# Kernel tuning notes

Measured on AMD Instinct MI355X. Metric: run time of the kernel, lower is better.

The kernel has to match this reference:

```python
import jax, jax.numpy as jnp
import numpy as np

B, N, D, H, DK = 4, 2048, 1024, 16, 64  # batch, seq, model_dim, heads, key_dim (= value_dim)
NEG = -1e9


def setup_inputs() -> dict:
    key = jax.random.key(0)
    ks = jax.random.split(key, 5)
    X = jax.random.normal(ks[0], (B, N, D), dtype=jnp.float32)
    # causal additive mask [N, N]; module slices mask[:N, :M] and adds to logits
    mask = jnp.where(jnp.tril(jnp.ones((N, N), dtype=bool)), 0.0, NEG).astype(jnp.float32)
    s = 1.0 / np.sqrt(D)
    Wq = jax.random.normal(ks[1], (D, H * DK), dtype=jnp.float32) * s
    Wk = jax.random.normal(ks[2], (D, H * DK), dtype=jnp.float32) * s
    Wv = jax.random.normal(ks[3], (D, H * DK), dtype=jnp.float32) * s
    Wo = jax.random.normal(ks[4], (H * DK, D), dtype=jnp.float32) * s
    return {"X": X, "mask": mask, "Wq": Wq, "Wk": Wk, "Wv": Wv, "Wo": Wo}


def reference(X, mask, Wq, Wk, Wv, Wo):
    # Linear projections (bias=False), then split heads: [B,N,H,DK] -> [B,H,N,DK]
    Q = (X @ Wq).reshape(B, N, H, DK).transpose(0, 2, 1, 3)
    K = (X @ Wk).reshape(B, N, H, DK).transpose(0, 2, 1, 3)
    V = (X @ Wv).reshape(B, N, H, DK).transpose(0, 2, 1, 3)
    # full [B,H,N,N] attention logits (module materializes it explicitly)
    att = jnp.einsum('bhnd,bhmd->bhnm', Q, K) / jnp.sqrt(jnp.float32(DK))
    # dropout is in eval mode here -> identity; then additive mask[:N,:M]
    att = att + mask[:N, :N]
    prob = jax.nn.softmax(att, axis=-1)
    values = jnp.einsum('bhnm,bhmd->bhnd', prob, V)
    values_cat = values.transpose(0, 2, 1, 3).reshape(B, N, H * DK)
    return values_cat @ Wo
```

## Files before the change

### kernel.cpp

```cpp
#include <hip/hip_runtime.h>

typedef __fp16   f2  __attribute__((ext_vector_type(2)));
typedef _Float16 h4  __attribute__((ext_vector_type(4)));
typedef _Float16 v8h __attribute__((ext_vector_type(8)));
typedef float    v4f __attribute__((ext_vector_type(4)));
struct f2x2 { f2 lo, hi; };

#if __has_builtin(__builtin_amdgcn_exp2f)
#define FEXP2(x) __builtin_amdgcn_exp2f(x)
#else
#define FEXP2(x) exp2f(x)
#endif

constexpr int Bn = 4, Nn = 2048, Dn = 1024, Hn = 16, DKn = 64, Mn = 8192;

__device__ __forceinline__ void load_lds16(const _Float16* g, _Float16* l) {
    __builtin_amdgcn_global_load_lds(
        (const __attribute__((address_space(1))) void*)g,
        (__attribute__((address_space(3))) void*)l, 16, 0, 0);
}

__global__ __launch_bounds__(256) void castAll(const float* __restrict__ x,
                                               _Float16* __restrict__ y,
                                               const float* __restrict__ Wq,
                                               const float* __restrict__ Wk,
                                               const float* __restrict__ Wv,
                                               const float* __restrict__ Wo,
                                               _Float16* __restrict__ Wqkv,
                                               _Float16* __restrict__ Wto) {
    __shared__ float tile[32][33];
    const int t = threadIdx.x;
    if (blockIdx.x < 8192) {
        const int i = blockIdx.x * 256 + t;
        const float4 v = ((const float4*)x)[i];
        h4 o; o[0] = (_Float16)v.x; o[1] = (_Float16)v.y;
        o[2] = (_Float16)v.z; o[3] = (_Float16)v.w;
        ((h4*)y)[i] = o;
        return;
    }
    const int wb = blockIdx.x - 8192;
    const int which = wb >> 10, bid = wb & 1023;
    const float* W = which == 0 ? Wq : which == 1 ? Wk : which == 2 ? Wv : Wo;
    _Float16* Dst = which < 3 ? (Wqkv + ((size_t)which << 20)) : Wto;
    const int bx = bid & 31, by = bid >> 5;
    const int r = t >> 3, c4 = (t & 7) * 4;
    const float4 v = *(const float4*)&W[(size_t)(by * 32 + r) * Dn + bx * 32 + c4];
    tile[r][c4 + 0] = v.x; tile[r][c4 + 1] = v.y;
    tile[r][c4 + 2] = v.z; tile[r][c4 + 3] = v.w;
    __syncthreads();
    h4 o;
    o[0] = (_Float16)tile[c4 + 0][r];
    o[1] = (_Float16)tile[c4 + 1][r];
    o[2] = (_Float16)tile[c4 + 2][r];
    o[3] = (_Float16)tile[c4 + 3][r];
    *(h4*)&Dst[(size_t)(bx * 32 + r) * Dn + by * 32 + c4] = o;
}

#define MFMA16(A, B, C) __builtin_amdgcn_mfma_f32_16x16x32_f16((A), (B), (C), 0, 0, 0)

__global__ __launch_bounds__(512, 2) void gemmqkv(const _Float16* __restrict__ A,
                                                  const _Float16* __restrict__ Wt,
                                                  _Float16* __restrict__ Qo,
                                                  _Float16* __restrict__ Ko,
                                                  _Float16* __restrict__ Vo)
{
    __shared__ __align__(16) _Float16 As[4 * 8192];
    __shared__ __align__(16) _Float16 Bs[4 * 6144];
    const int wgid = (blockIdx.x & 7) * 64 + (blockIdx.x >> 3);
    const int bx = wgid & 15, by = wgid >> 4;
    const int m0 = by * 256, n0 = bx * 192;
    const _Float16* Abase = A + (size_t)m0 * Dn;
    const _Float16* Bbase = Wt + (size_t)n0 * Dn;

    const int t = threadIdx.x, lane = t & 63, w = t >> 6;
    const int quad = lane >> 4, l16 = lane & 15;
    const int wm = w >> 2, wn = w & 3;
    const int rA = t >> 2;
    const int gc = ((t & 3) ^ ((t >> 3) & 3)) * 8;
    const _Float16* pA0 = Abase + (size_t)rA * Dn + gc;
    const _Float16* pA1 = pA0 + (size_t)128 * Dn;
    const _Float16* pB0 = Bbase + (size_t)rA * Dn + gc;
    const _Float16* pB1 = pB0 + (size_t)128 * Dn;
    auto stageA = [&](int ts, int sh) {
        const int reg = (ts & 1) * 2 + sh, ko = ts * 64 + sh * 32;
        load_lds16(pA0 + ko, As + reg * 8192 + w * 512);
        load_lds16(pA1 + ko, As + reg * 8192 + 4096 + w * 512);
    };
    auto stageB = [&](int ts, int sh) {
        const int reg = (ts & 1) * 2 + sh, ko = ts * 64 + sh * 32;
        load_lds16(pB0 + ko, Bs + reg * 6144 + w * 512);
        if (t < 256)
            load_lds16(pB1 + ko, Bs + reg * 6144 + 4096 + w * 512);
    };
    const int swz  = (quad ^ ((l16 >> 1) & 3)) * 8;
    const int aoff = (wm * 128 + l16) * 32 + swz;
    const int boff = (wn * 48 + l16) * 32 + swz;

    v4f acc[8][3];
#pragma unroll
    for (int i = 0; i < 8; ++i)
#pragma unroll
        for (int j = 0; j < 3; ++j) acc[i][j] = v4f{0.f, 0.f, 0.f, 0.f};

    stageA(0, 0); stageB(0, 0); stageA(0, 1); stageB(0, 1); stageA(1, 0); stageB(1, 0);
    asm volatile("s_waitcnt vmcnt(6)" ::: "memory");
    __builtin_amdgcn_s_barrier();

#define QKV_KSTEP(REG, TS, SH, DOST, VM, DOVM) do {                              \
    const _Float16* Ab_ = As + (REG) * 8192 + aoff;                              \
    const _Float16* Bb_ = Bs + (REG) * 6144 + boff;                              \
    v8h aL[4], aH[4], bL[3];                                                     \
    _Pragma("unroll") for (int q2 = 0; q2 < 4; ++q2)                             \
        aL[q2] = *(const v8h*)(Ab_ + q2 * 512);                                  \
    _Pragma("unroll") for (int q2 = 0; q2 < 3; ++q2)                             \
        bL[q2] = *(const v8h*)(Bb_ + q2 * 512);                                  \
    if (DOST) stageA((TS), (SH));                                                \
    __builtin_amdgcn_s_barrier();                                                \
    asm volatile("s_waitcnt lgkmcnt(0)" ::: "memory");                           \
    __builtin_amdgcn_s_setprio(1);                                               \
    _Pragma("unroll") for (int i2 = 0; i2 < 4; ++i2)                             \
        _Pragma("unroll") for (int j2 = 0; j2 < 3; ++j2)                         \
            acc[i2][j2] = MFMA16(aL[i2], bL[j2], acc[i2][j2]);                   \
    __builtin_amdgcn_s_setprio(0);                                               \
    __builtin_amdgcn_s_barrier();                                                \
    _Pragma("unroll") for (int q2 = 0; q2 < 4; ++q2)                             \
        aH[q2] = *(const v8h*)(Ab_ + 2048 + q2 * 512);                           \
    if (DOST) stageB((TS), (SH));                                                \
    __builtin_amdgcn_s_barrier();                                                \
    asm volatile("s_waitcnt lgkmcnt(0)" ::: "memory");                           \
    __builtin_amdgcn_s_setprio(1);                                               \
    _Pragma("unroll") for (int i2 = 0; i2 < 4; ++i2)                             \
        _Pragma("unroll") for (int j2 = 0; j2 < 3; ++j2)                         \
            acc[4 + i2][j2] = MFMA16(aH[i2], bL[j2], acc[4 + i2][j2]);           \
    __builtin_amdgcn_s_setprio(0);                                               \
    if (DOVM) asm volatile("s_waitcnt " VM ::: "memory");                        \
    __builtin_amdgcn_s_barrier();                                                \
} while (0)

    for (int tt = 0; tt < 14; tt += 2) {
        QKV_KSTEP(0, tt + 1, 1, true, "vmcnt(6)", true);
        QKV_KSTEP(1, tt + 2, 0, true, "vmcnt(6)", true);
        QKV_KSTEP(2, tt + 2, 1, true, "vmcnt(6)", true);
        QKV_KSTEP(3, tt + 3, 0, true, "vmcnt(6)", true);
    }
    QKV_KSTEP(0, 15, 1, true,  "vmcnt(6)", true);
    QKV_KSTEP(1, 0, 0, false, "vmcnt(3)", true);
    QKV_KSTEP(2, 0, 0, false, "vmcnt(0)", true);
    QKV_KSTEP(3, 0, 0, false, "vmcnt(0)", false);
#undef QKV_KSTEP

#pragma unroll
    for (int mf = 0; mf < 8; ++mf) {
        const int mbase = m0 + wm * 128 + mf * 16 + quad * 4;
        const int b = mbase >> 11, nr = mbase & (Nn - 1);
#pragma unroll
        for (int nf = 0; nf < 3; ++nf) {
            const int nG = n0 + wn * 48 + nf * 16 + l16;
            const int sec = nG >> 10, nl = nG & 1023;
            const int h = nl >> 6, dk = nl & 63;
            if (sec < 2) {
                _Float16* C = sec ? Ko : Qo;
                const float scale = sec ? 1.0f : 0.125f * 1.44269504f;
#pragma unroll
                for (int r = 0; r < 4; ++r)
                    C[((size_t)(b * Hn + h) * Nn + (nr + r)) * DKn + dk] =
                        (_Float16)(acc[mf][nf][r] * scale);
            } else {
                h4 o; o[0] = (_Float16)acc[mf][nf][0]; o[1] = (_Float16)acc[mf][nf][1];
                o[2] = (_Float16)acc[mf][nf][2]; o[3] = (_Float16)acc[mf][nf][3];
                *(h4*)&Vo[((size_t)(b * Hn + h) * DKn + dk) * Nn + nr] = o;
            }
        }
    }
}

__global__ __launch_bounds__(512, 2) void gemmo(const _Float16* __restrict__ A,
                                                const _Float16* __restrict__ Wt,
                                                float* __restrict__ C)
{
    __shared__ __align__(16) _Float16 As[4 * 8192];
    __shared__ __align__(16) _Float16 Bs[4 * 4096];
    const int wgid = (blockIdx.x & 7) * 32 + (blockIdx.x >> 3);
    const int bx = wgid & 7, by = wgid >> 3;
    const int m0 = by * 256, n0 = bx * 128;
    const _Float16* Abase = A + (size_t)m0 * Dn;
    const _Float16* Bbase = Wt + (size_t)n0 * Dn;

    const int t = threadIdx.x, lane = t & 63, w = t >> 6;
    const int quad = lane >> 4, l16 = lane & 15;
    const int wm = w & 3, wn = w >> 2;
    const int rA = t >> 2;
    const int gc = ((t & 3) ^ ((t >> 3) & 3)) * 8;
    const _Float16* pA0 = Abase + (size_t)rA * Dn + gc;
    const _Float16* pA1 = pA0 + (size_t)128 * Dn;
    const _Float16* pB0 = Bbase + (size_t)rA * Dn + gc;
    auto stage3 = [&](int ts, int sh) {
        const int reg = (ts & 1) * 2 + sh, ko = ts * 64 + sh * 32;
        load_lds16(pA0 + ko, As + reg * 8192 + w * 512);
        load_lds16(pA1 + ko, As + reg * 8192 + 4096 + w * 512);
        load_lds16(pB0 + ko, Bs + reg * 4096 + w * 512);
    };
    const int swz  = (quad ^ ((l16 >> 1) & 3)) * 8;
    const int aoff = (wm * 64 + l16) * 32 + swz;
    const int boff = (wn * 64 + l16) * 32 + swz;

    v4f acc[4][4];
#pragma unroll
    for (int i = 0; i < 4; ++i)
#pragma unroll
        for (int j = 0; j < 4; ++j) acc[i][j] = v4f{0.f, 0.f, 0.f, 0.f};

    stage3(0, 0); stage3(0, 1); stage3(1, 0);
    asm volatile("s_waitcnt vmcnt(6)" ::: "memory");
    __builtin_amdgcn_s_barrier();

#define O_KSTEP(REG, TS, SH, DOST, VM, DOVM) do {                                \
    const _Float16* Ab_ = As + (REG) * 8192 + aoff;                              \
    const _Float16* Bb_ = Bs + (REG) * 4096 + boff;                              \
    v8h aL[4], bL[4];                                                            \
    _Pragma("unroll") for (int q2 = 0; q2 < 4; ++q2) {                           \
        aL[q2] = *(const v8h*)(Ab_ + q2 * 512);                                  \
        bL[q2] = *(const v8h*)(Bb_ + q2 * 512);                                  \
    }                                                                            \
    if (DOST) stage3((TS), (SH));                                                \
    __builtin_amdgcn_s_barrier();                                                \
    asm volatile("s_waitcnt lgkmcnt(0)" ::: "memory");                           \
    __builtin_amdgcn_s_setprio(1);                                               \
    _Pragma("unroll") for (int i2 = 0; i2 < 4; ++i2)                             \
        _Pragma("unroll") for (int j2 = 0; j2 < 4; ++j2)                         \
            acc[i2][j2] = MFMA16(aL[i2], bL[j2], acc[i2][j2]);                   \
    __builtin_amdgcn_s_setprio(0);                                               \
    if (DOVM) asm volatile("s_waitcnt " VM ::: "memory");                        \
    __builtin_amdgcn_s_barrier();                                                \
} while (0)

    for (int tt = 0; tt < 14; tt += 2) {
        O_KSTEP(0, tt + 1, 1, true, "vmcnt(6)", true);
        O_KSTEP(1, tt + 2, 0, true, "vmcnt(6)", true);
        O_KSTEP(2, tt + 2, 1, true, "vmcnt(6)", true);
        O_KSTEP(3, tt + 3, 0, true, "vmcnt(6)", true);
    }
    O_KSTEP(0, 15, 1, true,  "vmcnt(6)", true);
    O_KSTEP(1, 0, 0, false, "vmcnt(3)", true);
    O_KSTEP(2, 0, 0, false, "vmcnt(0)", true);
    O_KSTEP(3, 0, 0, false, "vmcnt(0)", false);
#undef O_KSTEP

#pragma unroll
    for (int mf = 0; mf < 4; ++mf) {
        const int mbase = m0 + wm * 64 + mf * 16 + quad * 4;
#pragma unroll
        for (int nf = 0; nf < 4; ++nf) {
            const int n = n0 + wn * 64 + nf * 16 + l16;
#pragma unroll
            for (int r = 0; r < 4; ++r)
                C[(size_t)(mbase + r) * Dn + n] = acc[mf][nf][r];
        }
    }
}

__global__ __launch_bounds__(256) void flashv5(const _Float16* __restrict__ Q,
                                               const _Float16* __restrict__ K,
                                               const _Float16* __restrict__ Vt,
                                               _Float16* __restrict__ O)
{
    __shared__ __align__(16) _Float16 KS[64 * 64];
    __shared__ __align__(16) _Float16 VS[64 * 64];
    __shared__ __align__(16) _Float16 Ps[4][32 * 64];

    const int t = threadIdx.x;
    const int lane = t & 63, w = t >> 6;
    const int quad = lane >> 4, l16 = lane & 15;
    const int bh = blockIdx.x & 63;
    const int pr = blockIdx.x >> 6;
    const int b = bh >> 4, h = bh & 15;

    const _Float16* Qg = Q  + (size_t)bh * Nn * DKn;
    const _Float16* Kg = K  + (size_t)bh * Nn * DKn;
    const _Float16* Vg = Vt + (size_t)bh * DKn * Nn;

    auto stage = [&](int kt) {
        const int k0 = kt * 64;
#pragma unroll
        for (int jj = 0; jj < 2; ++jj) {
            const int ci = jj * 256 + w * 64 + lane;
            const int r = ci >> 3, c = ci & 7;
            const int gc = (c ^ (r & 7)) * 8;
            load_lds16(Kg + (size_t)(k0 + r) * DKn + gc, &KS[(jj * 256 + w * 64) * 8]);
            load_lds16(Vg + (size_t)r * Nn + k0 + gc,    &VS[(jj * 256 + w * 64) * 8]);
        }
    };
#define SWZ(arr, r, c) (*(const v8h*)&(arr)[(r) * 64 + (((c) ^ ((r) & 7)) * 8)])

    v8h ones;
#pragma unroll
    for (int i = 0; i < 8; ++i) ones[i] = (_Float16)1.0f;

    _Float16* Op = O + (size_t)b * Nn * Dn + h * DKn;

    for (int pass = 0; pass < 2; ++pass) {
        const int qtile = pass ? pr : 15 - pr;
        const int qb = qtile * 128 + w * 32;

        v8h qf[2][2];
#pragma unroll
        for (int qq = 0; qq < 2; ++qq)
#pragma unroll
            for (int ks = 0; ks < 2; ++ks)
                qf[qq][ks] = *(const v8h*)&Qg[(size_t)(qb + qq * 16 + l16) * DKn + ks * 32 + quad * 8];

        v4f o[2][4];
#pragma unroll
        for (int mq = 0; mq < 2; ++mq)
#pragma unroll
            for (int nt = 0; nt < 4; ++nt) o[mq][nt] = v4f{0.f, 0.f, 0.f, 0.f};
        v4f ol[2] = {v4f{0.f, 0.f, 0.f, 0.f}, v4f{0.f, 0.f, 0.f, 0.f}};

        const int NKT  = 2 * qtile + 2;
        const int diag = 2 * qtile + (w >> 1);

        for (int kt = 0; kt < NKT; ++kt) {
            stage(kt);
            __syncthreads();
            if (kt <= diag) {
                const int k0 = kt * 64;
                auto ptile = [&](bool domask) {
#pragma unroll
                    for (int kk = 0; kk < 4; ++kk) {
                        v4f s0 = v4f{0.f, 0.f, 0.f, 0.f}, s1 = v4f{0.f, 0.f, 0.f, 0.f};
#pragma unroll
                        for (int ks = 0; ks < 2; ++ks) {
                            const v8h ak = SWZ(KS, kk * 16 + l16, ks * 4 + quad);
                            s0 = __builtin_amdgcn_mfma_f32_16x16x32_f16(ak, qf[0][ks], s0, 0, 0, 0);
                            s1 = __builtin_amdgcn_mfma_f32_16x16x32_f16(ak, qf[1][ks], s1, 0, 0, 0);
                        }
                        const int key0 = k0 + kk * 16 + quad * 4;
#pragma unroll
                        for (int qq = 0; qq < 2; ++qq) {
                            const v4f sv = qq ? s1 : s0;
                            const int q = qb + qq * 16 + l16;
                            float p[4];
#pragma unroll
                            for (int r = 0; r < 4; ++r) {
                                float x = sv[r];
                                if (domask) x = (key0 + r > q) ? -1e9f : x;
                                p[r] = FEXP2(x);
                            }
                            f2x2 pkr;
                            pkr.lo = __builtin_amdgcn_cvt_pkrtz(p[0], p[1]);
                            pkr.hi = __builtin_amdgcn_cvt_pkrtz(p[2], p[3]);
                            const h4 pk = __builtin_bit_cast(h4, pkr);
                            const int prow = qq * 16 + l16;
                            const int pch  = kk * 2 + (quad >> 1);
                            *(h4*)&Ps[w][prow * 64 + ((pch ^ (prow & 7)) * 8 + (quad & 1) * 4)] = pk;
                        }
                    }
#pragma unroll
                    for (int ks = 0; ks < 2; ++ks)
#pragma unroll
                        for (int mq = 0; mq < 2; ++mq) {
                            const int arow = mq * 16 + l16;
                            const int ach  = ks * 4 + quad;
                            const v8h a = *(const v8h*)&Ps[w][arow * 64 + ((ach ^ (arow & 7)) * 8)];
#pragma unroll
                            for (int nt = 0; nt < 4; ++nt) {
                                const v8h bvv = SWZ(VS, nt * 16 + l16, ks * 4 + quad);
                                o[mq][nt] = __builtin_amdgcn_mfma_f32_16x16x32_f16(a, bvv, o[mq][nt], 0, 0, 0);
                            }
                            ol[mq] = __builtin_amdgcn_mfma_f32_16x16x32_f16(a, ones, ol[mq], 0, 0, 0);
                        }
                };
                if (kt == diag) ptile(true); else ptile(false);
            }
            __syncthreads();
        }

#pragma unroll
        for (int mq = 0; mq < 2; ++mq)
#pragma unroll
            for (int r = 0; r < 4; ++r) {
                const float li = 1.0f / ol[mq][r];
                const int qrow = qb + mq * 16 + quad * 4 + r;
#pragma unroll
                for (int nt = 0; nt < 4; ++nt)
                    Op[(size_t)qrow * Dn + nt * 16 + l16] = (_Float16)(o[mq][nt][r] * li);
            }
    }
#undef SWZ
}

extern "C" void kernel_launch(void* const* d_in, const int* in_sizes, int n_in,
                              void* d_out, int out_size, void* d_ws, size_t ws_size,
                              hipStream_t stream)
{
    const float* X  = (const float*)d_in[0];
    const float* Wq = (const float*)d_in[2];
    const float* Wk = (const float*)d_in[3];
    const float* Wv = (const float*)d_in[4];
    const float* Wo = (const float*)d_in[5];

    char* ws = (char*)d_ws;
    _Float16* Xh   = (_Float16*)ws;
    _Float16* Wqkv = (_Float16*)(ws + (16u << 20));
    _Float16* Wto  = Wqkv + (3u << 20);
    _Float16* Qh   = Wto + (1u << 20);
    _Float16* Kh   = Qh + (size_t)Mn * Dn;
    _Float16* Vth  = Kh + (size_t)Mn * Dn;
    _Float16* Ah   = Vth + (size_t)Mn * Dn;

    castAll<<<12288, 256, 0, stream>>>(X, Xh, Wq, Wk, Wv, Wo, Wqkv, Wto);
    gemmqkv<<<512, 512, 0, stream>>>(Xh, Wqkv, Qh, Kh, Vth);
    flashv5<<<512, 256, 0, stream>>>(Qh, Kh, Vth, Ah);
    gemmo<<<256, 512, 0, stream>>>(Ah, Wto, (float*)d_out);
}
```

Measured before the change: 249.1 us.

## Double-buffer K/V tiles in flash attention with async LDS prefetch

Splits the K and V shared-memory tiles into two buffers and issues the global-to-LDS loads for the next key tile before computing on the current one. Partial vmcnt waits and raw barriers replace the full __syncthreads pair, so memory latency can overlap with the MFMA work. This doubles the K/V LDS footprint, which may lower occupancy. The hand-written waitcnt counts assume exactly four outstanding loads per stage.

```diff
diff --git a/kernel.cpp b/kernel.cpp
--- a/kernel.cpp
+++ b/kernel.cpp
@@ -264,8 +264,8 @@
                                                const _Float16* __restrict__ Vt,
                                                _Float16* __restrict__ O)
 {
-    __shared__ __align__(16) _Float16 KS[64 * 64];
-    __shared__ __align__(16) _Float16 VS[64 * 64];
+    __shared__ __align__(16) _Float16 KS[2][64 * 64];
+    __shared__ __align__(16) _Float16 VS[2][64 * 64];
     __shared__ __align__(16) _Float16 Ps[4][32 * 64];
 
     const int t = threadIdx.x;
@@ -279,15 +279,15 @@
     const _Float16* Kg = K  + (size_t)bh * Nn * DKn;
     const _Float16* Vg = Vt + (size_t)bh * DKn * Nn;
 
-    auto stage = [&](int kt) {
+    auto stage = [&](int kt, int buf) {
         const int k0 = kt * 64;
 #pragma unroll
         for (int jj = 0; jj < 2; ++jj) {
             const int ci = jj * 256 + w * 64 + lane;
             const int r = ci >> 3, c = ci & 7;
             const int gc = (c ^ (r & 7)) * 8;
-            load_lds16(Kg + (size_t)(k0 + r) * DKn + gc, &KS[(jj * 256 + w * 64) * 8]);
-            load_lds16(Vg + (size_t)r * Nn + k0 + gc,    &VS[(jj * 256 + w * 64) * 8]);
+            load_lds16(Kg + (size_t)(k0 + r) * DKn + gc, &KS[buf][(jj * 256 + w * 64) * 8]);
+            load_lds16(Vg + (size_t)r * Nn + k0 + gc,    &VS[buf][(jj * 256 + w * 64) * 8]);
         }
     };
 #define SWZ(arr, r, c) (*(const v8h*)&(arr)[(r) * 64 + (((c) ^ ((r) & 7)) * 8)])
@@ -319,18 +319,27 @@
         const int NKT  = 2 * qtile + 2;
         const int diag = 2 * qtile + (w >> 1);
 
+        stage(0, 0);
         for (int kt = 0; kt < NKT; ++kt) {
-            stage(kt);
-            __syncthreads();
+            const int cur = kt & 1;
+            if (kt + 1 < NKT) {
+                stage(kt + 1, cur ^ 1);
+                asm volatile("s_waitcnt vmcnt(4)" ::: "memory");
+            } else {
+                asm volatile("s_waitcnt vmcnt(0)" ::: "memory");
+            }
+            __builtin_amdgcn_s_barrier();
             if (kt <= diag) {
                 const int k0 = kt * 64;
+                const _Float16* KSc = KS[cur];
+                const _Float16* VSc = VS[cur];
                 auto ptile = [&](bool domask) {
 #pragma unroll
                     for (int kk = 0; kk < 4; ++kk) {
                         v4f s0 = v4f{0.f, 0.f, 0.f, 0.f}, s1 = v4f{0.f, 0.f, 0.f, 0.f};
 #pragma unroll
                         for (int ks = 0; ks < 2; ++ks) {
-                            const v8h ak = SWZ(KS, kk * 16 + l16, ks * 4 + quad);
+                            const v8h ak = SWZ(KSc, kk * 16 + l16, ks * 4 + quad);
                             s0 = __builtin_amdgcn_mfma_f32_16x16x32_f16(ak, qf[0][ks], s0, 0, 0, 0);
                             s1 = __builtin_amdgcn_mfma_f32_16x16x32_f16(ak, qf[1][ks], s1, 0, 0, 0);
                         }
@@ -364,7 +373,7 @@
                             const v8h a = *(const v8h*)&Ps[w][arow * 64 + ((ach ^ (arow & 7)) * 8)];
 #pragma unroll
                             for (int nt = 0; nt < 4; ++nt) {
-                                const v8h bvv = SWZ(VS, nt * 16 + l16, ks * 4 + quad);
+                                const v8h bvv = SWZ(VSc, nt * 16 + l16, ks * 4 + quad);
                                 o[mq][nt] = __builtin_amdgcn_mfma_f32_16x16x32_f16(a, bvv, o[mq][nt], 0, 0, 0);
                             }
                             ol[mq] = __builtin_amdgcn_mfma_f32_16x16x32_f16(a, ones, ol[mq], 0, 0, 0);
@@ -372,7 +381,8 @@
                 };
                 if (kt == diag) ptile(true); else ptile(false);
             }
-            __syncthreads();
+            asm volatile("" ::: "memory");
+            __builtin_amdgcn_s_barrier();
         }
 
 #pragma unroll
```

After: 263.1 us. 1.06x slower.
